# Optimization experiments

Measured on AMD Instinct MI355X. Metric: run time of the kernel, lower is better.

The kernel has to match this reference:

```python
import jax, jax.numpy as jnp
import numpy as np

IN_DIM = 512
REDUCED = IN_DIM // 8  # reduction_ratio = 8
B, C, H, W = 8, 32, 64, IN_DIM


def setup_inputs() -> dict:
    key = jax.random.key(0)
    ks = jax.random.split(key, 9)
    s_in = 1.0 / np.sqrt(IN_DIM)
    inp = {
        "x": jax.random.normal(ks[0], (B, C, H, W), dtype=jnp.float32),
        # torch Linear weights stored here as [in, out] for y = x @ w + b
        "wq": jax.random.uniform(ks[1], (IN_DIM, REDUCED), jnp.float32, -s_in, s_in),
        "bq": jax.random.uniform(ks[2], (REDUCED,), jnp.float32, -s_in, s_in),
        "wk": jax.random.uniform(ks[3], (IN_DIM, REDUCED), jnp.float32, -s_in, s_in),
        "bk": jax.random.uniform(ks[4], (REDUCED,), jnp.float32, -s_in, s_in),
        "wv": jax.random.uniform(ks[5], (IN_DIM, IN_DIM), jnp.float32, -s_in, s_in),
        "bv": jax.random.uniform(ks[6], (IN_DIM,), jnp.float32, -s_in, s_in),
        "wo": jax.random.uniform(ks[7], (IN_DIM, IN_DIM), jnp.float32, -s_in, s_in),
        "bo": jax.random.uniform(ks[8], (IN_DIM,), jnp.float32, -s_in, s_in),
    }
    return inp


def reference(x, wq, bq, wk, bk, wv, bv, wo, bo):
    b, c, h, w = x.shape
    n = c * h  # attention tokens = flattened C*H positions, feature dim = W
    q = (x @ wq + bq).reshape(b, n, REDUCED)   # [B, N, r]
    k = (x @ wk + bk).reshape(b, n, REDUCED)   # [B, N, r]
    v = (x @ wv + bv).reshape(b, n, w)         # [B, N, W]
    energy = jnp.einsum("bnr,bmr->bnm", q, k)  # [B, N, N]
    attn = jax.nn.softmax(energy, axis=-1)
    out = jnp.einsum("bnm,bmd->bnd", attn, v).reshape(b, c, h, w)
    out = out @ wo + bo
    return out + x
```

## Files before the change

kernel.cpp:

```cpp
#include <hip/hip_runtime.h>

typedef __bf16 bf16x8 __attribute__((ext_vector_type(8)));
typedef float  f32x4  __attribute__((ext_vector_type(4)));

union U8 { uint4 v; unsigned short u[8]; };

static __device__ __forceinline__ float bf2f(unsigned short u) {
    union { unsigned int i; float f; } c; c.i = ((unsigned int)u) << 16; return c.f;
}
static __device__ __forceinline__ unsigned short f2bf(float f) {
    union { float f; unsigned int i; } c; c.f = f;
    unsigned int x = c.i;
    unsigned int r = (x + 0x7FFFu + ((x >> 16) & 1u)) >> 16;
    return (unsigned short)r;
}

static __device__ __forceinline__ U8 load8(const float* p) {
    U8 r;
    const float4 a = *(const float4*)p;
    const float4 b = *(const float4*)(p + 4);
    r.u[0] = f2bf(a.x); r.u[1] = f2bf(a.y); r.u[2] = f2bf(a.z); r.u[3] = f2bf(a.w);
    r.u[4] = f2bf(b.x); r.u[5] = f2bf(b.y); r.u[6] = f2bf(b.z); r.u[7] = f2bf(b.w);
    return r;
}

static __device__ __forceinline__ void gld_lds16(const void* g, void* l) {
    __builtin_amdgcn_global_load_lds(
        (const __attribute__((address_space(1))) unsigned int*)g,
        (__attribute__((address_space(3))) unsigned int*)l, 16, 0, 0);
}

__global__ __launch_bounds__(256)
void xconv(const float* __restrict__ x, unsigned short* __restrict__ xb,
           const float* __restrict__ bq, const float* __restrict__ bk,
           float* __restrict__ bqk)
{
    const long i = ((long)blockIdx.x * 256 + threadIdx.x) * 16;
    U8 a = load8(x + i);
    U8 b = load8(x + i + 8);
    *(uint4*)(xb + i) = a.v;
    *(uint4*)(xb + i + 8) = b.v;
    if (blockIdx.x == 0 && threadIdx.x < 128)
        bqk[threadIdx.x] = threadIdx.x < 64 ? bq[threadIdx.x] : bk[threadIdx.x - 64];
}

__global__ __launch_bounds__(256)
void transW(const float* __restrict__ wv, const float* __restrict__ wo,
            const float* __restrict__ wq, const float* __restrict__ wk,
            unsigned short* __restrict__ wvT, unsigned short* __restrict__ woT,
            unsigned short* __restrict__ wqkT)
{
    __shared__ float sT[64][65];
    const int zz = blockIdx.z;
    const float* src; unsigned short* dst; int C;
    if      (zz == 0) { src = wv; dst = wvT;            C = 512; }
    else if (zz == 1) { src = wo; dst = woT;            C = 512; }
    else if (zz == 2) { src = wq; dst = wqkT;           C = 64;  }
    else              { src = wk; dst = wqkT + 64*512;  C = 64;  }
    const int R = 512;
    const int c0 = blockIdx.x * 64, r0 = blockIdx.y * 64;
    if (c0 >= C) return;
    const int t = threadIdx.x;
    #pragma unroll
    for (int k = 0; k < 16; ++k) {
        const int lin = k * 256 + t;
        const int i = lin >> 6, j = lin & 63;
        sT[i][j] = src[(long)(r0 + i) * C + c0 + j];
    }
    __syncthreads();
    #pragma unroll
    for (int k = 0; k < 16; ++k) {
        const int lin = k * 256 + t;
        const int o = lin >> 6, i2 = lin & 63;
        dst[(long)(c0 + o) * R + r0 + i2] = f2bf(sT[i2][o]);
    }
}

template<bool BIAS, bool RES, bool OUT_F32, bool TRANSC>
__global__ __launch_bounds__(256, 4)
void gemm128(const unsigned short* __restrict__ A, int lda,
             const unsigned short* __restrict__ B, int ldb,
             void* __restrict__ Cp, int ldc,
             const float* __restrict__ bias,
             const float* __restrict__ resid,
             int K)
{
    __shared__ __align__(16) unsigned short sA[128 * 64];
    __shared__ __align__(16) unsigned short sB[128 * 64];

    const int t = threadIdx.x, wave = t >> 6, lane = t & 63;
    const int lr = lane & 15, quad = lane >> 4;
    const int rowBase = blockIdx.y * 128, colBase = blockIdx.x * 128;
    const int wm = (wave >> 1) * 64, wn = (wave & 1) * 64;

    const int srow  = lane >> 3;
    const int sslot = lane & 7;

    f32x4 acc[4][4];
    #pragma unroll
    for (int mt = 0; mt < 4; ++mt)
        #pragma unroll
        for (int nt = 0; nt < 4; ++nt) acc[mt][nt] = (f32x4){0.f, 0.f, 0.f, 0.f};

    for (int kt = 0; kt < K; kt += 64) {
        #pragma unroll
        for (int is = 0; is < 4; ++is) {
            const int r0  = wave * 32 + is * 8;
            const int row = r0 + srow;
            const int swz = (sslot ^ (row & 7)) << 4;
            gld_lds16((const char*)A + ((long)(rowBase + row) * lda + kt) * 2 + swz,
                      (char*)sA + r0 * 128);
            gld_lds16((const char*)B + ((long)(colBase + row) * ldb + kt) * 2 + swz,
                      (char*)sB + r0 * 128);
        }
        __syncthreads();

        #pragma unroll
        for (int ks = 0; ks < 2; ++ks) {
            const int kb = ks * 64 + quad * 16;
            bf16x8 bfr[4];
            #pragma unroll
            for (int nt = 0; nt < 4; ++nt) {
                const int row = wn + nt * 16 + lr;
                bfr[nt] = *(const bf16x8*)((const char*)sB + row * 128 + (kb ^ ((row & 7) << 4)));
            }
            #pragma unroll
            for (int mt = 0; mt < 4; ++mt) {
                const int row = wm + mt * 16 + lr;
                bf16x8 af = *(const bf16x8*)((const char*)sA + row * 128 + (kb ^ ((row & 7) << 4)));
                #pragma unroll
                for (int nt = 0; nt < 4; ++nt)
                    acc[mt][nt] = __builtin_amdgcn_mfma_f32_16x16x32_bf16(af, bfr[nt], acc[mt][nt], 0, 0, 0);
            }
        }
        __syncthreads();
    }

    float* Cf = (float*)Cp;
    unsigned short* Cb = (unsigned short*)Cp;
    #pragma unroll
    for (int mt = 0; mt < 4; ++mt)
        #pragma unroll
        for (int nt = 0; nt < 4; ++nt) {
            const int row0 = rowBase + wm + mt * 16 + quad * 4;
            const int col  = colBase + wn + nt * 16 + lr;
            if (TRANSC) {
                const int bat = row0 >> 11, key = row0 & 2047;
                const float b = BIAS ? bias[col] : 0.f;
                ushort4 v4;
                v4.x = f2bf(acc[mt][nt][0] + b);
                v4.y = f2bf(acc[mt][nt][1] + b);
                v4.z = f2bf(acc[mt][nt][2] + b);
                v4.w = f2bf(acc[mt][nt][3] + b);
                *(ushort4*)&Cb[((long)bat * 512 + col) * 2048 + key] = v4;
            } else {
                const float b = BIAS ? bias[col] : 0.f;
                #pragma unroll
                for (int r = 0; r < 4; ++r) {
                    const int row = row0 + r;
                    float v = acc[mt][nt][r] + b;
                    if (RES)     v += resid[(long)row * ldc + col];
                    if (OUT_F32) Cf[(long)row * ldc + col] = v;
                    else         Cb[(long)row * ldc + col] = f2bf(v);
                }
            }
        }
}

__global__ __launch_bounds__(256, 4)
void flash_attn(const unsigned short* __restrict__ QK,
                const unsigned short* __restrict__ VT,
                unsigned short* __restrict__ O)
{
    __shared__ __align__(16) unsigned short sK[2][64 * 64];
    __shared__ __align__(16) unsigned short sP[2][64 * 72];
    __shared__ float sL[64];

    const int bid = blockIdx.x;
    const int z  = bid & 7;
    const int rr = bid >> 3;
    const int cs = rr & 3;
    const int qt = rr >> 2;

    const int t = threadIdx.x, wave = t >> 6, lane = t & 63;
    const int lr = lane & 15, quad = lane >> 4;

    const long qrow0 = (long)z * 2048 + qt * 64;
    const unsigned short* qp = QK + (qrow0 + wave * 16 + lr) * 128 + quad * 8;
    const bf16x8 qa0 = *(const bf16x8*)(qp);
    const bf16x8 qa1 = *(const bf16x8*)(qp + 32);

    const char* Kb = (const char*)(QK + (long)z * 2048 * 128 + 64);
    const unsigned short* Vb = VT + (long)z * 512 * 2048
                                  + ((long)cs * 128 + wave * 32) * 2048;

    const long stg_go = (long)(wave * 16 + (lane >> 3)) * 256
                      + (((lane & 7) ^ (lane >> 3)) << 4);
    const int swq = (lr & 7) << 4;

    f32x4 acc[4][2];
    #pragma unroll
    for (int mt = 0; mt < 4; ++mt)
        #pragma unroll
        for (int nt = 0; nt < 2; ++nt) acc[mt][nt] = (f32x4){0.f, 0.f, 0.f, 0.f};
    float lsum[4] = {0.f, 0.f, 0.f, 0.f};

    {
        const char* gk = Kb + stg_go;
        char* lk = (char*)sK[0] + wave * 2048;
        gld_lds16(gk, lk);
        gld_lds16(gk + 2048, lk + 1024);
    }
    __syncthreads();

    int cur = 0;
    for (int kt = 0; kt < 32; ++kt) {
        const int key0 = kt * 64;

        bf16x8 vv[2][2];
        #pragma unroll
        for (int nt = 0; nt < 2; ++nt) {
            const unsigned short* vp = Vb + (long)(nt * 16 + lr) * 2048 + key0 + quad * 8;
            vv[nt][0] = *(const bf16x8*)(vp);
            vv[nt][1] = *(const bf16x8*)(vp + 32);
        }

        if (kt < 31) {
            const char* gk = Kb + (long)(kt + 1) * 64 * 256 + stg_go;
            char* lk = (char*)sK[cur ^ 1] + wave * 2048;
            gld_lds16(gk, lk);
            gld_lds16(gk + 2048, lk + 1024);
        }

        const char* sKc = (const char*)sK[cur];
        f32x4 s[4];
        #pragma unroll
        for (int nt = 0; nt < 4; ++nt) {
            const int kb = (nt * 16 + lr) * 128;
            bf16x8 k0 = *(const bf16x8*)(sKc + kb + ((quad * 16) ^ swq));
            bf16x8 k1 = *(const bf16x8*)(sKc + kb + ((quad * 16 + 64) ^ swq));
            f32x4 sv = (f32x4){0.f, 0.f, 0.f, 0.f};
            sv = __builtin_amdgcn_mfma_f32_16x16x32_bf16(qa0, k0, sv, 0, 0, 0);
            sv = __builtin_amdgcn_mfma_f32_16x16x32_bf16(qa1, k1, sv, 0, 0, 0);
            s[nt] = sv;
        }

        unsigned short* sPc = sP[cur];
        #pragma unroll
        for (int nt = 0; nt < 4; ++nt)
            #pragma unroll
            for (int r = 0; r < 4; ++r) {
                const float e = __expf(s[nt][r]);
                const unsigned short pb = f2bf(e);
                lsum[r] += bf2f(pb);
                sPc[(wave * 16 + quad * 4 + r) * 72 + nt * 16 + lr] = pb;
            }

        __syncthreads();

        #pragma unroll
        for (int mt = 0; mt < 4; ++mt) {
            const unsigned short* pp = &sPc[(mt * 16 + lr) * 72 + quad * 8];
            bf16x8 p0 = *(const bf16x8*)(pp);
            bf16x8 p1 = *(const bf16x8*)(pp + 32);
            acc[mt][0] = __builtin_amdgcn_mfma_f32_16x16x32_bf16(p0, vv[0][0], acc[mt][0], 0, 0, 0);
            acc[mt][0] = __builtin_amdgcn_mfma_f32_16x16x32_bf16(p1, vv[0][1], acc[mt][0], 0, 0, 0);
            acc[mt][1] = __builtin_amdgcn_mfma_f32_16x16x32_bf16(p0, vv[1][0], acc[mt][1], 0, 0, 0);
            acc[mt][1] = __builtin_amdgcn_mfma_f32_16x16x32_bf16(p1, vv[1][1], acc[mt][1], 0, 0, 0);
        }
        cur ^= 1;
    }

    #pragma unroll
    for (int r = 0; r < 4; ++r) {
        float v = lsum[r];
        v += __shfl_xor(v, 1); v += __shfl_xor(v, 2);
        v += __shfl_xor(v, 4); v += __shfl_xor(v, 8);
        lsum[r] = v;
    }
    if (lr == 0) {
        #pragma unroll
        for (int r = 0; r < 4; ++r) sL[wave * 16 + quad * 4 + r] = lsum[r];
    }
    __syncthreads();

    #pragma unroll
    for (int mt = 0; mt < 4; ++mt) {
        float inv[4];
        #pragma unroll
        for (int r = 0; r < 4; ++r) inv[r] = 1.0f / sL[mt * 16 + quad * 4 + r];
        #pragma unroll
        for (int nt = 0; nt < 2; ++nt) {
            const int col = cs * 128 + wave * 32 + nt * 16 + lr;
            #pragma unroll
            for (int r = 0; r < 4; ++r) {
                const long row = qrow0 + mt * 16 + quad * 4 + r;
                O[row * 512 + col] = f2bf(acc[mt][nt][r] * inv[r]);
            }
        }
    }
}

extern "C" void kernel_launch(void* const* d_in, const int* in_sizes, int n_in,
                              void* d_out, int out_size, void* d_ws, size_t ws_size,
                              hipStream_t stream)
{
    const float* x  = (const float*)d_in[0];
    const float* wq = (const float*)d_in[1];
    const float* bq = (const float*)d_in[2];
    const float* wk = (const float*)d_in[3];
    const float* bk = (const float*)d_in[4];
    const float* wv = (const float*)d_in[5];
    const float* bv = (const float*)d_in[6];
    const float* wo = (const float*)d_in[7];
    const float* bo = (const float*)d_in[8];

    const int W = 512;
    float* out = (float*)d_out;
    dim3 blk(256);
    char* ws = (char*)d_ws;

    const size_t NEED = 56ull << 20;
    if (ws_size < NEED) return;

    unsigned short* QK   = (unsigned short*)(ws);
    unsigned short* VT   = (unsigned short*)(ws + ( 4ull << 20));
    unsigned short* O    = (unsigned short*)(ws + (20ull << 20));
    unsigned short* xb   = (unsigned short*)(ws + (36ull << 20));
    unsigned short* wvT  = (unsigned short*)(ws + (52ull << 20));
    unsigned short* woT  = (unsigned short*)(ws + (52ull << 20) + (512ull << 10));
    unsigned short* wqkT = (unsigned short*)(ws + (53ull << 20));
    float*          bqk  = (float*)         (ws + (53ull << 20) + (256ull << 10));

    xconv<<<dim3(2048), blk, 0, stream>>>(x, xb, bq, bk, bqk);
    transW<<<dim3(8, 8, 4), blk, 0, stream>>>(wv, wo, wq, wk, wvT, woT, wqkT);

    gemm128<true, false, false, false><<<dim3(1, 128), blk, 0, stream>>>(
        xb, W, wqkT, W, QK, 128, bqk, nullptr, W);
    gemm128<true, false, false, true><<<dim3(4, 128), blk, 0, stream>>>(
        xb, W, wvT, W, VT, 0, bv, nullptr, W);

    flash_attn<<<dim3(1024), blk, 0, stream>>>(QK, VT, O);

    gemm128<true, true, true, false><<<dim3(4, 128), blk, 0, stream>>>(
        O, W, woT, W, out, W, bo, x, W);
}
```

Before: 222.7 us.

## Fuse prep kernels, merge QK/V projections, and retile flash attention to 32 rows

Merges the x-to-bf16 conversion and the weight transposes into one pack kernel. Concatenates Wq, Wk and Wv so one GEMM launch produces both the QK buffer and the transposed V, which removes two launches and a second read of x. Flash attention now uses 32 query rows per block with waves split across key halves and 256 output columns each. This halves the redundant QK^T and softmax work per output column and raises the PV MFMA density, at the cost of more V registers and two partial row sums. It also adds s_setprio around the MFMA block.

```diff
diff --git a/kernel.cpp b/kernel.cpp
--- a/kernel.cpp
+++ b/kernel.cpp
@@ -31,36 +31,39 @@
 }
 
 __global__ __launch_bounds__(256)
-void xconv(const float* __restrict__ x, unsigned short* __restrict__ xb,
-           const float* __restrict__ bq, const float* __restrict__ bk,
-           float* __restrict__ bqk)
+void pack(const float* __restrict__ x, unsigned short* __restrict__ xb,
+          const float* __restrict__ bq, const float* __restrict__ bk,
+          const float* __restrict__ bv, float* __restrict__ ball,
+          const float* __restrict__ wv, const float* __restrict__ wo,
+          const float* __restrict__ wq, const float* __restrict__ wk,
+          unsigned short* __restrict__ wAllT, unsigned short* __restrict__ woT)
 {
-    const long i = ((long)blockIdx.x * 256 + threadIdx.x) * 16;
-    U8 a = load8(x + i);
-    U8 b = load8(x + i + 8);
-    *(uint4*)(xb + i) = a.v;
-    *(uint4*)(xb + i + 8) = b.v;
-    if (blockIdx.x == 0 && threadIdx.x < 128)
-        bqk[threadIdx.x] = threadIdx.x < 64 ? bq[threadIdx.x] : bk[threadIdx.x - 64];
-}
-
-__global__ __launch_bounds__(256)
-void transW(const float* __restrict__ wv, const float* __restrict__ wo,
-            const float* __restrict__ wq, const float* __restrict__ wk,
-            unsigned short* __restrict__ wvT, unsigned short* __restrict__ woT,
-            unsigned short* __restrict__ wqkT)
-{
+    const int bid = blockIdx.x, t = threadIdx.x;
+    if (bid < 2048) {
+        const long i = ((long)bid * 256 + t) * 16;
+        U8 a = load8(x + i);
+        U8 b = load8(x + i + 8);
+        *(uint4*)(xb + i) = a.v;
+        *(uint4*)(xb + i + 8) = b.v;
+        if (bid == 0) {
+            ball[t]       = t < 64 ? bq[t] : (t < 128 ? bk[t - 64] : bv[t - 128]);
+            ball[t + 256] = bv[t + 128];
+            if (t < 128) ball[t + 512] = bv[t + 384];
+        }
+        return;
+    }
     __shared__ float sT[64][65];
-    const int zz = blockIdx.z;
+    const int b2 = bid - 2048;
+    const int zz = b2 >> 6, rem = b2 & 63;
+    const int cx = rem & 7, ry = rem >> 3;
     const float* src; unsigned short* dst; int C;
-    if      (zz == 0) { src = wv; dst = wvT;            C = 512; }
-    else if (zz == 1) { src = wo; dst = woT;            C = 512; }
-    else if (zz == 2) { src = wq; dst = wqkT;           C = 64;  }
-    else              { src = wk; dst = wqkT + 64*512;  C = 64;  }
+    if      (zz == 0) { src = wv; dst = wAllT + 128 * 512; C = 512; }
+    else if (zz == 1) { src = wo; dst = woT;               C = 512; }
+    else if (zz == 2) { src = wq; dst = wAllT;             C = 64;  }
+    else              { src = wk; dst = wAllT + 64 * 512;  C = 64;  }
     const int R = 512;
-    const int c0 = blockIdx.x * 64, r0 = blockIdx.y * 64;
+    const int c0 = cx * 64, r0 = ry * 64;
     if (c0 >= C) return;
-    const int t = threadIdx.x;
     #pragma unroll
     for (int k = 0; k < 16; ++k) {
         const int lin = k * 256 + t;
@@ -76,11 +79,12 @@
     }
 }
 
-template<bool BIAS, bool RES, bool OUT_F32, bool TRANSC>
+template<bool BIAS, bool RES, bool OUT_F32, bool TRANSC, bool MIXED>
 __global__ __launch_bounds__(256, 4)
 void gemm128(const unsigned short* __restrict__ A, int lda,
              const unsigned short* __restrict__ B, int ldb,
              void* __restrict__ Cp, int ldc,
+             void* __restrict__ Cp2,
              const float* __restrict__ bias,
              const float* __restrict__ resid,
              int K)
@@ -138,23 +142,31 @@
 
     float* Cf = (float*)Cp;
     unsigned short* Cb = (unsigned short*)Cp;
+    unsigned short* C2 = (unsigned short*)Cp2;
     #pragma unroll
     for (int mt = 0; mt < 4; ++mt)
         #pragma unroll
         for (int nt = 0; nt < 4; ++nt) {
             const int row0 = rowBase + wm + mt * 16 + quad * 4;
             const int col  = colBase + wn + nt * 16 + lr;
-            if (TRANSC) {
+            const float b = BIAS ? bias[col] : 0.f;
+            if (MIXED && colBase >= 128) {
                 const int bat = row0 >> 11, key = row0 & 2047;
-                const float b = BIAS ? bias[col] : 0.f;
                 ushort4 v4;
                 v4.x = f2bf(acc[mt][nt][0] + b);
                 v4.y = f2bf(acc[mt][nt][1] + b);
                 v4.z = f2bf(acc[mt][nt][2] + b);
                 v4.w = f2bf(acc[mt][nt][3] + b);
-                *(ushort4*)&Cb[((long)bat * 512 + col) * 2048 + key] = v4;
+                *(ushort4*)&C2[((long)bat * 512 + (col - 128)) * 2048 + key] = v4;
+            } else if (TRANSC) {
+                const int bat = row0 >> 11, key = row0 & 2047;
+                ushort4 v4;
+                v4.x = f2bf(acc[mt][nt][0] + b);
+                v4.y = f2bf(acc[mt][nt][1] + b);
+                v4.z = f2bf(acc[mt][nt][2] + b);
+                v4.w = f2bf(acc[mt][nt][3] + b);
+                *(ushort4*)&C2[((long)bat * 512 + col) * 2048 + key] = v4;
             } else {
-                const float b = BIAS ? bias[col] : 0.f;
                 #pragma unroll
                 for (int r = 0; r < 4; ++r) {
                     const int row = row0 + r;
@@ -173,36 +185,38 @@
                 unsigned short* __restrict__ O)
 {
     __shared__ __align__(16) unsigned short sK[2][64 * 64];
-    __shared__ __align__(16) unsigned short sP[2][64 * 72];
-    __shared__ float sL[64];
+    __shared__ __align__(16) unsigned short sP[2][32 * 72];
+    __shared__ float sL[2][32];
 
     const int bid = blockIdx.x;
     const int z  = bid & 7;
     const int rr = bid >> 3;
-    const int cs = rr & 3;
-    const int qt = rr >> 2;
+    const int cs = rr & 1;
+    const int qt = rr >> 1;
 
     const int t = threadIdx.x, wave = t >> 6, lane = t & 63;
     const int lr = lane & 15, quad = lane >> 4;
-
-    const long qrow0 = (long)z * 2048 + qt * 64;
-    const unsigned short* qp = QK + (qrow0 + wave * 16 + lr) * 128 + quad * 8;
+    const int srg = wave & 1;
+    const int skg = wave >> 1;
+
+    const long qrow0 = (long)z * 2048 + qt * 32;
+    const unsigned short* qp = QK + (qrow0 + srg * 16 + lr) * 128 + quad * 8;
     const bf16x8 qa0 = *(const bf16x8*)(qp);
     const bf16x8 qa1 = *(const bf16x8*)(qp + 32);
 
     const char* Kb = (const char*)(QK + (long)z * 2048 * 128 + 64);
     const unsigned short* Vb = VT + (long)z * 512 * 2048
-                                  + ((long)cs * 128 + wave * 32) * 2048;
+                                  + ((long)cs * 256 + wave * 64) * 2048;
 
     const long stg_go = (long)(wave * 16 + (lane >> 3)) * 256
                       + (((lane & 7) ^ (lane >> 3)) << 4);
     const int swq = (lr & 7) << 4;
 
-    f32x4 acc[4][2];
-    #pragma unroll
-    for (int mt = 0; mt < 4; ++mt)
-        #pragma unroll
-        for (int nt = 0; nt < 2; ++nt) acc[mt][nt] = (f32x4){0.f, 0.f, 0.f, 0.f};
+    f32x4 acc[2][4];
+    #pragma unroll
+    for (int mt = 0; mt < 2; ++mt)
+        #pragma unroll
+        for (int nt = 0; nt < 4; ++nt) acc[mt][nt] = (f32x4){0.f, 0.f, 0.f, 0.f};
     float lsum[4] = {0.f, 0.f, 0.f, 0.f};
 
     {
@@ -217,57 +231,60 @@
     for (int kt = 0; kt < 32; ++kt) {
         const int key0 = kt * 64;
 
-        bf16x8 vv[2][2];
-        #pragma unroll
-        for (int nt = 0; nt < 2; ++nt) {
+        bf16x8 vv[4][2];
+        #pragma unroll
+        for (int nt = 0; nt < 4; ++nt) {
             const unsigned short* vp = Vb + (long)(nt * 16 + lr) * 2048 + key0 + quad * 8;
             vv[nt][0] = *(const bf16x8*)(vp);
             vv[nt][1] = *(const bf16x8*)(vp + 32);
         }
 
         if (kt < 31) {
-            const char* gk = Kb + (long)(kt + 1) * 64 * 256 + stg_go;
+            const char* gk = Kb + (long)(kt + 1) * 16384 + stg_go;
             char* lk = (char*)sK[cur ^ 1] + wave * 2048;
             gld_lds16(gk, lk);
             gld_lds16(gk + 2048, lk + 1024);
         }
 
         const char* sKc = (const char*)sK[cur];
-        f32x4 s[4];
-        #pragma unroll
-        for (int nt = 0; nt < 4; ++nt) {
-            const int kb = (nt * 16 + lr) * 128;
+        __bf16* sPb = (__bf16*)sP[cur];
+        #pragma unroll
+        for (int g = 0; g < 2; ++g) {
+            const int key = skg * 32 + g * 16 + lr;
+            const int kb = key * 128;
             bf16x8 k0 = *(const bf16x8*)(sKc + kb + ((quad * 16) ^ swq));
             bf16x8 k1 = *(const bf16x8*)(sKc + kb + ((quad * 16 + 64) ^ swq));
             f32x4 sv = (f32x4){0.f, 0.f, 0.f, 0.f};
             sv = __builtin_amdgcn_mfma_f32_16x16x32_bf16(qa0, k0, sv, 0, 0, 0);
             sv = __builtin_amdgcn_mfma_f32_16x16x32_bf16(qa1, k1, sv, 0, 0, 0);
-            s[nt] = sv;
-        }
-
-        unsigned short* sPc = sP[cur];
-        #pragma unroll
-        for (int nt = 0; nt < 4; ++nt)
             #pragma unroll
             for (int r = 0; r < 4; ++r) {
-                const float e = __expf(s[nt][r]);
-                const unsigned short pb = f2bf(e);
-                lsum[r] += bf2f(pb);
-                sPc[(wave * 16 + quad * 4 + r) * 72 + nt * 16 + lr] = pb;
-            }
+                const float e = __expf(sv[r]);
+                const __bf16 pb = (__bf16)e;
+                lsum[r] += (float)pb;
+                sPb[(srg * 16 + quad * 4 + r) * 72 + skg * 32 + g * 16 + lr] = pb;
+            }
+        }
 
         __syncthreads();
 
-        #pragma unroll
-        for (int mt = 0; mt < 4; ++mt) {
-            const unsigned short* pp = &sPc[(mt * 16 + lr) * 72 + quad * 8];
-            bf16x8 p0 = *(const bf16x8*)(pp);
-            bf16x8 p1 = *(const bf16x8*)(pp + 32);
-            acc[mt][0] = __builtin_amdgcn_mfma_f32_16x16x32_bf16(p0, vv[0][0], acc[mt][0], 0, 0, 0);
-            acc[mt][0] = __builtin_amdgcn_mfma_f32_16x16x32_bf16(p1, vv[0][1], acc[mt][0], 0, 0, 0);
-            acc[mt][1] = __builtin_amdgcn_mfma_f32_16x16x32_bf16(p0, vv[1][0], acc[mt][1], 0, 0, 0);
-            acc[mt][1] = __builtin_amdgcn_mfma_f32_16x16x32_bf16(p1, vv[1][1], acc[mt][1], 0, 0, 0);
-        }
+        const char* sPc = (const char*)sP[cur];
+        bf16x8 p[2][2];
+        #pragma unroll
+        for (int mt = 0; mt < 2; ++mt) {
+            const char* pp = sPc + (mt * 16 + lr) * 144 + quad * 16;
+            p[mt][0] = *(const bf16x8*)(pp);
+            p[mt][1] = *(const bf16x8*)(pp + 64);
+        }
+        __builtin_amdgcn_s_setprio(1);
+        #pragma unroll
+        for (int mt = 0; mt < 2; ++mt)
+            #pragma unroll
+            for (int nt = 0; nt < 4; ++nt) {
+                acc[mt][nt] = __builtin_amdgcn_mfma_f32_16x16x32_bf16(p[mt][0], vv[nt][0], acc[mt][nt], 0, 0, 0);
+                acc[mt][nt] = __builtin_amdgcn_mfma_f32_16x16x32_bf16(p[mt][1], vv[nt][1], acc[mt][nt], 0, 0, 0);
+            }
+        __builtin_amdgcn_s_setprio(0);
         cur ^= 1;
     }
 
@@ -280,18 +297,21 @@
     }
     if (lr == 0) {
         #pragma unroll
-        for (int r = 0; r < 4; ++r) sL[wave * 16 + quad * 4 + r] = lsum[r];
+        for (int r = 0; r < 4; ++r) sL[skg][srg * 16 + quad * 4 + r] = lsum[r];
     }
     __syncthreads();
 
     #pragma unroll
-    for (int mt = 0; mt < 4; ++mt) {
+    for (int mt = 0; mt < 2; ++mt) {
         float inv[4];
         #pragma unroll
-        for (int r = 0; r < 4; ++r) inv[r] = 1.0f / sL[mt * 16 + quad * 4 + r];
-        #pragma unroll
-        for (int nt = 0; nt < 2; ++nt) {
-            const int col = cs * 128 + wave * 32 + nt * 16 + lr;
+        for (int r = 0; r < 4; ++r) {
+            const int rl = mt * 16 + quad * 4 + r;
+            inv[r] = 1.0f / (sL[0][rl] + sL[1][rl]);
+        }
+        #pragma unroll
+        for (int nt = 0; nt < 4; ++nt) {
+            const int col = cs * 256 + wave * 64 + nt * 16 + lr;
             #pragma unroll
             for (int r = 0; r < 4; ++r) {
                 const long row = qrow0 + mt * 16 + quad * 4 + r;
@@ -323,25 +343,22 @@
     const size_t NEED = 56ull << 20;
     if (ws_size < NEED) return;
 
-    unsigned short* QK   = (unsigned short*)(ws);
-    unsigned short* VT   = (unsigned short*)(ws + ( 4ull << 20));
-    unsigned short* O    = (unsigned short*)(ws + (20ull << 20));
-    unsigned short* xb   = (unsigned short*)(ws + (36ull << 20));
-    unsigned short* wvT  = (unsigned short*)(ws + (52ull << 20));
-    unsigned short* woT  = (unsigned short*)(ws + (52ull << 20) + (512ull << 10));
-    unsigned short* wqkT = (unsigned short*)(ws + (53ull << 20));
-    float*          bqk  = (float*)         (ws + (53ull << 20) + (256ull << 10));
-
-    xconv<<<dim3(2048), blk, 0, stream>>>(x, xb, bq, bk, bqk);
-    transW<<<dim3(8, 8, 4), blk, 0, stream>>>(wv, wo, wq, wk, wvT, woT, wqkT);
-
-    gemm128<true, false, false, false><<<dim3(1, 128), blk, 0, stream>>>(
-        xb, W, wqkT, W, QK, 128, bqk, nullptr, W);
-    gemm128<true, false, false, true><<<dim3(4, 128), blk, 0, stream>>>(
-        xb, W, wvT, W, VT, 0, bv, nullptr, W);
+    unsigned short* QK    = (unsigned short*)(ws);
+    unsigned short* VT    = (unsigned short*)(ws + ( 4ull << 20));
+    unsigned short* O     = (unsigned short*)(ws + (20ull << 20));
+    unsigned short* xb    = (unsigned short*)(ws + (36ull << 20));
+    unsigned short* wAllT = (unsigned short*)(ws + (52ull << 20));
+    unsigned short* woT   = (unsigned short*)(ws + (53ull << 20));
+    float*          ball  = (float*)         (ws + (53ull << 20) + (512ull << 10));
+
+    pack<<<dim3(2048 + 256), blk, 0, stream>>>(x, xb, bq, bk, bv, ball,
+                                               wv, wo, wq, wk, wAllT, woT);
+
+    gemm128<true, false, false, false, true><<<dim3(5, 128), blk, 0, stream>>>(
+        xb, W, wAllT, W, QK, 128, VT, ball, nullptr, W);
 
     flash_attn<<<dim3(1024), blk, 0, stream>>>(QK, VT, O);
 
-    gemm128<true, true, true, false><<<dim3(4, 128), blk, 0, stream>>>(
-        O, W, woT, W, out, W, bo, x, W);
-}
+    gemm128<true, true, true, false, false><<<dim3(4, 128), blk, 0, stream>>>(
+        O, W, woT, W, out, W, nullptr, bo, x, W);
+}
```

Result: slower. 264.7 us (+18.8%).
